# Optimization experiments

Measured on AMD Instinct MI355X. Metric: run time of the kernel, lower is better.

Reference implementation:

```python
import jax, jax.numpy as jnp
import numpy as np

B, N, K = 4, 2048, 48
NUM_RBF = 16
NUM_PE = 16
MAX_REL = 32
EDGE_C = 128
PE_IN = 2 * MAX_REL + 2  # 66


def setup_inputs() -> dict:
    key = jax.random.key(0)
    ks = jax.random.split(key, 10)
    coords = jax.random.normal(ks[0], (B, N, 3), dtype=jnp.float32) * 10.0
    token_exists_mask = jnp.ones((B, N), dtype=jnp.float32)
    token_bonds = (jax.random.uniform(ks[1], (B, N, N)) < 0.01).astype(jnp.float32)
    pe_w = jax.random.normal(ks[2], (PE_IN, NUM_PE), dtype=jnp.float32) * 0.05
    pe_b = jnp.zeros((NUM_PE,), dtype=jnp.float32)
    edge_w = jax.random.normal(ks[3], (NUM_PE + NUM_RBF + 1, EDGE_C), dtype=jnp.float32) * 0.05
    ln_g = jnp.ones((EDGE_C,), dtype=jnp.float32)
    ln_b = jnp.zeros((EDGE_C,), dtype=jnp.float32)
    token_to_center_atom = jax.random.randint(ks[4], (B, N), 0, N, dtype=jnp.int32)
    residue_index = jnp.sort(jax.random.randint(ks[5], (B, N), 0, 4096, dtype=jnp.int32), axis=-1)
    asym_id = jax.random.randint(ks[6], (B, N), 0, 4, dtype=jnp.int32)
    is_ligand = jax.random.randint(ks[7], (B, N), 0, 2, dtype=jnp.int32)
    return {
        'coords': coords, 'token_exists_mask': token_exists_mask,
        'token_bonds': token_bonds, 'pe_w': pe_w, 'pe_b': pe_b,
        'edge_w': edge_w, 'ln_g': ln_g, 'ln_b': ln_b,
        'token_to_center_atom': token_to_center_atom,
        'residue_index': residue_index, 'asym_id': asym_id,
        'is_ligand': is_ligand,
    }


def _gather_edges(M, E_idx):
    # M: [B, N, N], E_idx: [B, N, K] -> [B, N, K]
    return jnp.take_along_axis(M, E_idx, axis=2)


def _rbf(D):
    # D: [..., K] -> [..., K, NUM_RBF]
    D_mu = jnp.linspace(2.0, 22.0, NUM_RBF)
    D_sigma = (22.0 - 2.0) / NUM_RBF
    return jnp.exp(-(((D[..., None] - D_mu) / D_sigma) ** 2))


def reference(coords, token_exists_mask, token_bonds, pe_w, pe_b, edge_w,
              ln_g, ln_b, token_to_center_atom, residue_index, asym_id, is_ligand):
    # token coords: center atom per token, masked
    X = jnp.take_along_axis(coords, token_to_center_atom[..., None], axis=1)
    X = X * token_exists_mask[..., None]  # [B, N, 3]

    # masked pairwise distances + KNN (smallest K, sorted ascending)
    mask = token_exists_mask
    mask_2d = mask[:, None, :] * mask[:, :, None]  # [B, N, N]
    dX = X[:, :, None, :] - X[:, None, :, :]
    D = mask_2d * jnp.sqrt(jnp.sum(dX * dX, axis=-1) + 1e-6)
    D_max = jnp.max(D, axis=-1, keepdims=True)
    D_adjust = D + (1.0 - mask_2d) * D_max
    neg_D, E_idx = jax.lax.top_k(-D_adjust, K)  # largest of -D == smallest of D
    D_neighbors = -neg_D  # [B, N, K]

    RBF_all = _rbf(D_neighbors)  # [B, N, K, NUM_RBF]

    # relative sequence position features
    offset = residue_index[:, :, None] - residue_index[:, None, :]  # [B, N, N]
    offset_e = _gather_edges(offset, E_idx)  # [B, N, K]
    chain_labels = jnp.zeros_like(asym_id)  # use_multichain_encoding=False
    d_chains = (chain_labels[:, :, None] - chain_labels[:, None, :] == 0).astype(jnp.int32)
    E_chains = _gather_edges(d_chains, E_idx)  # [B, N, K]
    d = jnp.clip(offset_e + MAX_REL, 0, 2 * MAX_REL) * E_chains + (1 - E_chains) * (2 * MAX_REL + 1)
    d_onehot = jax.nn.one_hot(d, PE_IN, dtype=jnp.float32)
    E_positional = d_onehot @ pe_w + pe_b  # [B, N, K, NUM_PE]

    # ligand-gated bond feature
    lig = is_ligand.astype(bool)
    tb_mask = (lig[:, :, None] | lig[:, None, :]).astype(token_bonds.dtype)
    tb = token_bonds * tb_mask
    tb_e = _gather_edges(tb, E_idx)[..., None]  # [B, N, K, 1]

    # fuse, embed, layernorm
    E = jnp.concatenate([E_positional, RBF_all, tb_e], axis=-1)  # [B, N, K, 33]
    E = E @ edge_w  # [B, N, K, EDGE_C]
    mu = jnp.mean(E, axis=-1, keepdims=True)
    var = jnp.mean((E - mu) ** 2, axis=-1, keepdims=True)
    E = (E - mu) / jnp.sqrt(var + 1e-5) * ln_g + ln_b
    return (E, E_idx, D_neighbors)
```

## Files before the change

kernel.cpp:

```cpp
#include <hip/hip_runtime.h>
#include <math.h>

namespace {
constexpr int B_ = 4;
constexpr int N_ = 2048;
constexpr int K_ = 48;
constexpr int MAX_REL_ = 32;
constexpr int EDGE_C_ = 128;
constexpr int NUM_PE_ = 16;
constexpr int NROWS = B_ * N_;
constexpr int NEDGE = NROWS * K_;
}

__global__ __launch_bounds__(256) void x_kernel(const float* __restrict__ coords,
                                                const float* __restrict__ mask,
                                                const int* __restrict__ t2ca,
                                                float* __restrict__ X) {
    int r = blockIdx.x * 256 + threadIdx.x;
    if (r >= NROWS) return;
    int b = r >> 11;
    int c = t2ca[r];
    float m = mask[r];
    const float* s = coords + ((size_t)(b * N_ + c)) * 3;
    X[r * 3 + 0] = __fmul_rn(s[0], m);
    X[r * 3 + 1] = __fmul_rn(s[1], m);
    X[r * 3 + 2] = __fmul_rn(s[2], m);
}

__global__ __launch_bounds__(256) void prep_a(const float* __restrict__ edge_w,
                                              const float* __restrict__ ln_g,
                                              float* __restrict__ Wcf,
                                              float* __restrict__ Wg) {
    __shared__ float sm[33];
    const int wv = threadIdx.x >> 6;
    const int lane = threadIdx.x & 63;
    for (int r = wv; r < 33; r += 4) {
        float v = edge_w[r * 128 + lane] + edge_w[r * 128 + 64 + lane];
        #pragma unroll
        for (int off = 32; off; off >>= 1) v += __shfl_xor(v, off, 64);
        if (lane == 0) sm[r] = v * (1.0f / 128.0f);
    }
    __syncthreads();
    for (int idx = threadIdx.x; idx < 33 * 128; idx += 256) {
        int p = idx >> 7, c = idx & 127;
        float cen = edge_w[idx] - sm[p];
        Wcf[idx] = cen;
        if (p >= 16) Wg[(p - 16) * 128 + c] = cen * ln_g[c];
    }
}

__global__ __launch_bounds__(128) void prep_b(const float* __restrict__ pe_w,
                                              const float* __restrict__ pe_b,
                                              const float* __restrict__ Wcf,
                                              const float* __restrict__ ln_g,
                                              float* __restrict__ C1c,
                                              float* __restrict__ C1g) {
    const int d = blockIdx.x, c = threadIdx.x;
    float acc = 0.0f;
    #pragma unroll
    for (int q = 0; q < 16; ++q)
        acc = fmaf(pe_w[d * 16 + q] + pe_b[q], Wcf[q * 128 + c], acc);
    C1c[d * 128 + c] = acc;
    C1g[d * 128 + c] = acc * ln_g[c];
}

__global__ __launch_bounds__(256) void prep_c(const float* __restrict__ Wcf,
                                              const float* __restrict__ C1c,
                                              float* __restrict__ V0,
                                              float* __restrict__ T12_2,
                                              float* __restrict__ Tb1_2,
                                              float* __restrict__ A22,
                                              float* __restrict__ A23_2,
                                              float* __restrict__ A33) {
    const int idx = blockIdx.x * 256 + threadIdx.x;
    const float* u; const float* v; float scale; float* dst;
    if (idx < 1040) {
        int d = idx >> 4, r = idx & 15;
        u = C1c + d * 128; v = Wcf + (16 + r) * 128;
        scale = 2.0f / 128.0f; dst = T12_2 + idx;
    } else if (idx < 1105) {
        int d = idx - 1040;
        u = C1c + d * 128; v = u; scale = 1.0f / 128.0f; dst = V0 + d;
    } else if (idx < 1170) {
        int d = idx - 1105;
        u = C1c + d * 128; v = Wcf + 32 * 128; scale = 2.0f / 128.0f; dst = Tb1_2 + d;
    } else if (idx < 1426) {
        int i = idx - 1170; int r = i >> 4, s = i & 15;
        u = Wcf + (16 + r) * 128; v = Wcf + (16 + s) * 128;
        scale = 1.0f / 128.0f; dst = A22 + i;
    } else if (idx < 1442) {
        int r = idx - 1426;
        u = Wcf + (16 + r) * 128; v = Wcf + 32 * 128;
        scale = 2.0f / 128.0f; dst = A23_2 + r;
    } else if (idx == 1442) {
        u = Wcf + 32 * 128; v = u; scale = 1.0f / 128.0f; dst = A33;
    } else return;
    float a = 0.0f;
    #pragma unroll 8
    for (int c = 0; c < 128; ++c) a = fmaf(u[c], v[c], a);
    *dst = a * scale;
}

__global__ __launch_bounds__(256) void knn_kernel(const float* __restrict__ X,
                                                  const float* __restrict__ mask,
                                                  float* __restrict__ eidx_f,
                                                  float* __restrict__ dneb) {
    __shared__ unsigned s_hist[4][256];
    __shared__ unsigned long long s_cbuf[4][64];
    const int wv = threadIdx.x >> 6;
    const int lane = threadIdx.x & 63;
    const int row = blockIdx.x * 4 + wv;
    const int b = row >> 11;

    const float xi0 = X[row * 3 + 0];
    const float xi1 = X[row * 3 + 1];
    const float xi2 = X[row * 3 + 2];
    const float mi = mask[row];
    const float* Xb = X + (size_t)b * N_ * 3;
    const float* mb = mask + b * N_;

    unsigned fb[32];
    float lmax = -INFINITY;
    #pragma unroll
    for (int t = 0; t < 32; ++t) {
        int j = t * 64 + lane;
        float dx = __fsub_rn(xi0, Xb[j * 3 + 0]);
        float dy = __fsub_rn(xi1, Xb[j * 3 + 1]);
        float dz = __fsub_rn(xi2, Xb[j * 3 + 2]);
        float d2 = __fmaf_rn(dz, dz, __fmaf_rn(dx, dx, __fmul_rn(dy, dy)));
        float m2 = __fmul_rn(mi, mb[j]);
        float dd = __fmul_rn(m2, __fsqrt_rn(__fadd_rn(d2, 1e-6f)));
        fb[t] = __float_as_uint(dd);
        lmax = fmaxf(lmax, dd);
    }
    #pragma unroll
    for (int off = 32; off; off >>= 1) lmax = fmaxf(lmax, __shfl_xor(lmax, off, 64));

    unsigned fmin_l = 0xFFFFFFFFu, fmax_l = 0u;
    #pragma unroll
    for (int t = 0; t < 32; ++t) {
        int j = t * 64 + lane;
        float m2 = __fmul_rn(mi, mb[j]);
        float adj = __fadd_rn(__uint_as_float(fb[t]),
                              __fmul_rn(__fsub_rn(1.0f, m2), lmax));
        unsigned u = __float_as_uint(adj);
        fb[t] = u;
        fmin_l = min(fmin_l, u);
        fmax_l = max(fmax_l, u);
    }
    #pragma unroll
    for (int off = 32; off; off >>= 1) {
        fmin_l = min(fmin_l, (unsigned)__shfl_xor((int)fmin_l, off, 64));
        fmax_l = max(fmax_l, (unsigned)__shfl_xor((int)fmax_l, off, 64));
    }
    const unsigned fminb = fmin_l;
    const unsigned range = fmax_l - fminb;
    const int vbits = (range == 0u) ? 0 : (32 - __clz((int)range));
    const int L = vbits + 11;
    int sh = (L > 8) ? (L - 8) : 0;

    unsigned cand = 0xFFFFFFFFu;
    int k_rem = K_;
    unsigned long long T = 0ull;

    while (true) {
        s_hist[wv][4 * lane + 0] = 0u;
        s_hist[wv][4 * lane + 1] = 0u;
        s_hist[wv][4 * lane + 2] = 0u;
        s_hist[wv][4 * lane + 3] = 0u;
        __asm__ volatile("s_waitcnt lgkmcnt(0)" ::: "memory");
        #pragma unroll
        for (int t = 0; t < 32; ++t) {
            if ((cand >> t) & 1u) {
                unsigned dig;
                if (sh >= 11) {
                    dig = ((fb[t] - fminb) >> (sh - 11)) & 255u;
                } else {
                    unsigned long long key =
                        ((unsigned long long)(fb[t] - fminb) << 11)
                        | (unsigned long long)(unsigned)(t * 64 + lane);
                    dig = (unsigned)(key >> sh) & 255u;
                }
                atomicAdd(&s_hist[wv][dig], 1u);
            }
        }
        __asm__ volatile("s_waitcnt lgkmcnt(0)" ::: "memory");
        const unsigned c0 = s_hist[wv][4 * lane + 0];
        const unsigned c1 = s_hist[wv][4 * lane + 1];
        const unsigned c2 = s_hist[wv][4 * lane + 2];
        const unsigned c3 = s_hist[wv][4 * lane + 3];
        const unsigned s4 = c0 + c1 + c2 + c3;
        unsigned inc = s4;
        #pragma unroll
        for (int off = 1; off < 64; off <<= 1) {
            unsigned o = (unsigned)__shfl_up((int)inc, off, 64);
            if (lane >= off) inc += o;
        }
        const unsigned ex = inc - s4;
        const unsigned e1 = ex + c0, e2 = e1 + c1, e3 = e2 + c2;
        const unsigned kr = (unsigned)k_rem;
        int digl = -1; unsigned below = 0u, bc = 0u;
        if (ex < kr && kr <= e1)           { digl = 4 * lane + 0; below = ex; bc = c0; }
        else if (e1 < kr && kr <= e2)      { digl = 4 * lane + 1; below = e1; bc = c1; }
        else if (e2 < kr && kr <= e3)      { digl = 4 * lane + 2; below = e2; bc = c2; }
        else if (e3 < kr && kr <= e3 + c3) { digl = 4 * lane + 3; below = e3; bc = c3; }

        unsigned long long bal = __ballot(digl >= 0);
        int src = __ffsll((long long)bal) - 1;
        const int dstar = __shfl(digl, src, 64);
        below = (unsigned)__shfl((int)below, src, 64);
        bc    = (unsigned)__shfl((int)bc, src, 64);
        k_rem -= (int)below;

        unsigned nc = 0u;
        unsigned long long myT = 0ull;
        #pragma unroll
        for (int t = 0; t < 32; ++t) {
            if ((cand >> t) & 1u) {
                unsigned dig;
                unsigned long long key =
                    ((unsigned long long)(fb[t] - fminb) << 11)
                    | (unsigned long long)(unsigned)(t * 64 + lane);
                if (sh >= 11) dig = ((fb[t] - fminb) >> (sh - 11)) & 255u;
                else          dig = (unsigned)(key >> sh) & 255u;
                if (dig == (unsigned)dstar) { nc |= (1u << t); myT = key; }
            }
        }
        cand = nc;
        if (bc == 1u || sh == 0) {
            unsigned long long b2 = __ballot(cand != 0u);
            int owner = __ffsll((long long)b2) - 1;
            T = __shfl(myT, owner, 64);
            break;
        }
        sh = (sh > 8) ? (sh - 8) : 0;
    }

    const unsigned Tv = (unsigned)(T >> 11);
    const unsigned Tj = (unsigned)(T & 2047u);
    unsigned selm = 0u; int scnt = 0;
    #pragma unroll
    for (int t = 0; t < 32; ++t) {
        unsigned v = fb[t] - fminb;
        unsigned j = (unsigned)(t * 64 + lane);
        if (v < Tv || (v == Tv && j <= Tj)) { selm |= (1u << t); ++scnt; }
    }
    int isc = scnt;
    #pragma unroll
    for (int off = 1; off < 64; off <<= 1) {
        int o = __shfl_up(isc, off, 64);
        if (lane >= off) isc += o;
    }
    int pos = isc - scnt;
    #pragma unroll
    for (int t = 0; t < 32; ++t) {
        if ((selm >> t) & 1u) {
            s_cbuf[wv][pos] = ((unsigned long long)(fb[t] - fminb) << 11)
                            | (unsigned long long)(unsigned)(t * 64 + lane);
            ++pos;
        }
    }
    __asm__ volatile("s_waitcnt lgkmcnt(0)" ::: "memory");
    unsigned long long kk = (lane < K_) ? s_cbuf[wv][lane] : ~0ull;

    #pragma unroll
    for (int k2 = 2; k2 <= 64; k2 <<= 1) {
        #pragma unroll
        for (int j = k2 >> 1; j > 0; j >>= 1) {
            unsigned long long o = __shfl_xor(kk, j, 64);
            const bool dirAsc = ((lane & k2) == 0);
            const bool lower = ((lane & j) == 0);
            unsigned long long mn = (kk < o) ? kk : o;
            unsigned long long mx = (kk < o) ? o : kk;
            kk = (lower == dirAsc) ? mn : mx;
        }
    }

    if (lane < K_) {
        unsigned fbits = (unsigned)(kk >> 11) + fminb;
        unsigned ji = (unsigned)(kk & 2047u);
        dneb[(size_t)row * K_ + lane] = __uint_as_float(fbits);
        eidx_f[(size_t)row * K_ + lane] = (float)ji;
    }
}

__global__ __launch_bounds__(256, 3) void edge_kernel(const float* __restrict__ eidx_f,
                                                      const float* __restrict__ dneb,
                                                      const float* __restrict__ token_bonds,
                                                      const float* __restrict__ C1g,
                                                      const float* __restrict__ Wg,
                                                      const float* __restrict__ V0,
                                                      const float* __restrict__ T12_2,
                                                      const float* __restrict__ Tb1_2,
                                                      const float* __restrict__ A22,
                                                      const float* __restrict__ A23_2,
                                                      const float* __restrict__ A33,
                                                      const float* __restrict__ ln_b,
                                                      const int* __restrict__ res_idx,
                                                      const int* __restrict__ is_lig,
                                                      float* __restrict__ Eout) {
    __shared__ float s_rbf[4][K_][20];
    __shared__ float4 s_meta[4][K_];
    __shared__ float s_D[4][K_];
    __shared__ float s_A22[256];
    __shared__ float s_A23[16];
    __shared__ float s_A33v;
    const int tid = threadIdx.x;
    const int wv = tid >> 6;
    const int lane = tid & 63;
    const int row = blockIdx.x * 4 + wv;
    const int b = row >> 11;

    s_A22[tid] = A22[tid];
    if (tid < 16) s_A23[tid] = A23_2[tid];
    if (tid == 0) s_A33v = A33[0];

    const int ri = res_idx[row];
    const int li = is_lig[row];

    int doff_l = 0; float tb_l = 0.0f;
    if (lane < K_) {
        const int e = row * K_ + lane;
        const int j = (int)(eidx_f[e] + 0.5f);
        const float D = dneb[e];
        const int jrow = b * N_ + j;
        const int rj = res_idx[jrow];
        const int lj = is_lig[jrow];
        float tb = token_bonds[(size_t)row * N_ + j];
        tb_l = (li | lj) ? tb : 0.0f;
        doff_l = min(max(ri - rj + MAX_REL_, 0), 2 * MAX_REL_);
        s_D[wv][lane] = D;
    }
    __syncthreads();

    #pragma unroll
    for (int t = 0; t < (K_ * NUM_PE_) / 64; ++t) {
        const int idx = t * 64 + lane;
        const int k = idx >> 4, r = idx & 15;
        const float D = s_D[wv][k];
        const float mu = 2.0f + (float)r * (4.0f / 3.0f);
        const float x = (D - mu) * 0.8f;
        s_rbf[wv][k][r] = __expf(-x * x);
    }
    __syncthreads();

    if (lane < K_) {
        float rr[16];
        const float* rb = &s_rbf[wv][lane][0];
        *(float4*)&rr[0]  = *(const float4*)&rb[0];
        *(float4*)&rr[4]  = *(const float4*)&rb[4];
        *(float4*)&rr[8]  = *(const float4*)&rb[8];
        *(float4*)&rr[12] = *(const float4*)&rb[12];
        float var = V0[doff_l];
        const float4* t12 = (const float4*)(T12_2 + doff_l * 16);
        float4 q0 = t12[0], q1 = t12[1], q2 = t12[2], q3 = t12[3];
        var = fmaf(rr[0], q0.x, var);  var = fmaf(rr[1], q0.y, var);
        var = fmaf(rr[2], q0.z, var);  var = fmaf(rr[3], q0.w, var);
        var = fmaf(rr[4], q1.x, var);  var = fmaf(rr[5], q1.y, var);
        var = fmaf(rr[6], q1.z, var);  var = fmaf(rr[7], q1.w, var);
        var = fmaf(rr[8], q2.x, var);  var = fmaf(rr[9], q2.y, var);
        var = fmaf(rr[10], q2.z, var); var = fmaf(rr[11], q2.w, var);
        var = fmaf(rr[12], q3.x, var); var = fmaf(rr[13], q3.y, var);
        var = fmaf(rr[14], q3.z, var); var = fmaf(rr[15], q3.w, var);
        #pragma unroll
        for (int r = 0; r < 16; ++r) {
            float tr = 0.0f;
            const float4* arow = (const float4*)&s_A22[r * 16];
            #pragma unroll
            for (int s4 = 0; s4 < 4; ++s4) {
                float4 a = arow[s4];
                tr = fmaf(rr[s4 * 4 + 0], a.x, tr);
                tr = fmaf(rr[s4 * 4 + 1], a.y, tr);
                tr = fmaf(rr[s4 * 4 + 2], a.z, tr);
                tr = fmaf(rr[s4 * 4 + 3], a.w, tr);
            }
            var = fmaf(rr[r], tr, var);
        }
        if (tb_l != 0.0f) {
            float extra = Tb1_2[doff_l];
            #pragma unroll
            for (int r = 0; r < 16; ++r) extra = fmaf(rr[r], s_A23[r], extra);
            var = fmaf(tb_l, extra, var);
            var = fmaf(tb_l * tb_l, s_A33v, var);
        }
        const float rstd = rsqrtf(var + 1e-5f);
        s_meta[wv][lane] = make_float4((float)doff_l, tb_l, rstd, 0.0f);
    }
    __syncthreads();

    const int hl = lane & 31;
    const int eo = lane >> 5;
    float4 wgt[17];
    #pragma unroll
    for (int p = 0; p < 17; ++p)
        wgt[p] = ((const float4*)Wg)[p * 32 + hl];
    const float4 bb = ((const float4*)ln_b)[hl];

    float4* outp = (float4*)Eout + (size_t)row * K_ * 32 + hl;
    #pragma unroll 2
    for (int k = 0; k < K_; k += 2) {
        const float4 mt = s_meta[wv][k + eo];
        const int doffk = (int)mt.x;
        const float tbk = mt.y;
        const float rstd = mt.z;
        const float4 c1 = ((const float4*)(C1g + ((size_t)doffk << 7)))[hl];

        float rr[16];
        const float* rb = &s_rbf[wv][k + eo][0];
        *(float4*)&rr[0]  = *(const float4*)&rb[0];
        *(float4*)&rr[4]  = *(const float4*)&rb[4];
        *(float4*)&rr[8]  = *(const float4*)&rb[8];
        *(float4*)&rr[12] = *(const float4*)&rb[12];

        float ax = c1.x, ay = c1.y, az = c1.z, aw = c1.w;
        #pragma unroll
        for (int p = 0; p < 16; ++p) {
            ax = fmaf(rr[p], wgt[p].x, ax);
            ay = fmaf(rr[p], wgt[p].y, ay);
            az = fmaf(rr[p], wgt[p].z, az);
            aw = fmaf(rr[p], wgt[p].w, aw);
        }
        if (__any(tbk != 0.0f)) {
            ax = fmaf(tbk, wgt[16].x, ax);
            ay = fmaf(tbk, wgt[16].y, ay);
            az = fmaf(tbk, wgt[16].z, az);
            aw = fmaf(tbk, wgt[16].w, aw);
        }
        float4 o;
        o.x = fmaf(ax, rstd, bb.x);
        o.y = fmaf(ay, rstd, bb.y);
        o.z = fmaf(az, rstd, bb.z);
        o.w = fmaf(aw, rstd, bb.w);
        outp[(size_t)(k + eo) * 32] = o;
    }
}

extern "C" void kernel_launch(void* const* d_in, const int* in_sizes, int n_in,
                              void* d_out, int out_size, void* d_ws, size_t ws_size,
                              hipStream_t stream) {
    const float* coords      = (const float*)d_in[0];
    const float* mask        = (const float*)d_in[1];
    const float* token_bonds = (const float*)d_in[2];
    const float* pe_w        = (const float*)d_in[3];
    const float* pe_b        = (const float*)d_in[4];
    const float* edge_w      = (const float*)d_in[5];
    const float* ln_g        = (const float*)d_in[6];
    const float* ln_b        = (const float*)d_in[7];
    const int*   t2ca        = (const int*)d_in[8];
    const int*   res_idx     = (const int*)d_in[9];
    const int*   is_lig      = (const int*)d_in[11];

    float* out    = (float*)d_out;
    float* Eout   = out;
    float* eidx_f = out + (size_t)NEDGE * EDGE_C_;
    float* dneb   = eidx_f + NEDGE;

    float* X     = (float*)d_ws;
    float* Wcf   = X + (size_t)NROWS * 3;
    float* Wg    = Wcf + 33 * 128;
    float* C1c   = Wg + 17 * 128;
    float* C1g   = C1c + 65 * 128;
    float* V0    = C1g + 65 * 128;
    float* T12_2 = V0 + 65;
    float* Tb1_2 = T12_2 + 65 * 16;
    float* A22   = Tb1_2 + 65;
    float* A23_2 = A22 + 256;
    float* A33   = A23_2 + 16;

    hipLaunchKernelGGL(x_kernel, dim3(NROWS / 256), dim3(256), 0, stream,
                       coords, mask, t2ca, X);
    hipLaunchKernelGGL(prep_a, dim3(1), dim3(256), 0, stream,
                       edge_w, ln_g, Wcf, Wg);
    hipLaunchKernelGGL(prep_b, dim3(65), dim3(128), 0, stream,
                       pe_w, pe_b, Wcf, ln_g, C1c, C1g);
    hipLaunchKernelGGL(prep_c, dim3(6), dim3(256), 0, stream,
                       Wcf, C1c, V0, T12_2, Tb1_2, A22, A23_2, A33);
    hipLaunchKernelGGL(knn_kernel, dim3(NROWS / 4), dim3(256), 0, stream,
                       X, mask, eidx_f, dneb);
    hipLaunchKernelGGL(edge_kernel, dim3(NROWS / 4), dim3(256), 0, stream,
                       eidx_f, dneb, token_bonds, C1g, Wg, V0, T12_2, Tb1_2,
                       A22, A23_2, A33, ln_b, res_idx, is_lig, Eout);
}
```

Before: 379.7 us.

## Fuse KNN and edge kernels, merge prep kernels, pack coords with mask

Merges the three single-purpose prep kernels into one single-block kernel that keeps the centered weights and positional products in shared memory. Fuses the KNN kernel with the edge embedding kernel so neighbour indices and distances stay in registers rather than being read back from global memory. Block-wide syncs are replaced by per-wave LDS waits, which is valid because each wave touches only its own row's shared slices. X is packed as float4 with the mask in .w, and the mask-adjust pass uses a bitmask instead of recomputing. The trade-off is a single-block prep kernel that may serialize, and higher register pressure in the fused kernel.

```diff
diff --git a/kernel.cpp b/kernel.cpp
--- a/kernel.cpp
+++ b/kernel.cpp
@@ -15,122 +15,139 @@
 __global__ __launch_bounds__(256) void x_kernel(const float* __restrict__ coords,
                                                 const float* __restrict__ mask,
                                                 const int* __restrict__ t2ca,
-                                                float* __restrict__ X) {
+                                                float4* __restrict__ X4) {
     int r = blockIdx.x * 256 + threadIdx.x;
     if (r >= NROWS) return;
     int b = r >> 11;
     int c = t2ca[r];
     float m = mask[r];
     const float* s = coords + ((size_t)(b * N_ + c)) * 3;
-    X[r * 3 + 0] = __fmul_rn(s[0], m);
-    X[r * 3 + 1] = __fmul_rn(s[1], m);
-    X[r * 3 + 2] = __fmul_rn(s[2], m);
+    X4[r] = make_float4(__fmul_rn(s[0], m), __fmul_rn(s[1], m),
+                        __fmul_rn(s[2], m), m);
 }
 
-__global__ __launch_bounds__(256) void prep_a(const float* __restrict__ edge_w,
-                                              const float* __restrict__ ln_g,
-                                              float* __restrict__ Wcf,
-                                              float* __restrict__ Wg) {
+__global__ __launch_bounds__(256) void prep_kernel(const float* __restrict__ pe_w,
+                                                   const float* __restrict__ pe_b,
+                                                   const float* __restrict__ edge_w,
+                                                   const float* __restrict__ ln_g,
+                                                   float* __restrict__ Wg,
+                                                   float* __restrict__ C1g,
+                                                   float* __restrict__ T12_2,
+                                                   float* __restrict__ A22,
+                                                   float* __restrict__ A23_2,
+                                                   float* __restrict__ V0,
+                                                   float* __restrict__ Tb1_2,
+                                                   float* __restrict__ A33) {
+    __shared__ float sW[33][129];
+    __shared__ float sC[65][129];
     __shared__ float sm[33];
-    const int wv = threadIdx.x >> 6;
-    const int lane = threadIdx.x & 63;
+    const int tid = threadIdx.x;
+    const int wv = tid >> 6;
+    const int lane = tid & 63;
+
+    for (int idx = tid; idx < 33 * 128; idx += 256)
+        sW[idx >> 7][idx & 127] = edge_w[idx];
+    __syncthreads();
     for (int r = wv; r < 33; r += 4) {
-        float v = edge_w[r * 128 + lane] + edge_w[r * 128 + 64 + lane];
+        float v = sW[r][lane] + sW[r][64 + lane];
         #pragma unroll
         for (int off = 32; off; off >>= 1) v += __shfl_xor(v, off, 64);
         if (lane == 0) sm[r] = v * (1.0f / 128.0f);
     }
     __syncthreads();
-    for (int idx = threadIdx.x; idx < 33 * 128; idx += 256) {
+    for (int idx = tid; idx < 33 * 128; idx += 256) {
         int p = idx >> 7, c = idx & 127;
-        float cen = edge_w[idx] - sm[p];
-        Wcf[idx] = cen;
+        float cen = sW[p][c] - sm[p];
+        sW[p][c] = cen;
         if (p >= 16) Wg[(p - 16) * 128 + c] = cen * ln_g[c];
     }
+    __syncthreads();
+    for (int idx = tid; idx < 65 * 128; idx += 256) {
+        int d = idx >> 7, c = idx & 127;
+        float acc = 0.0f;
+        #pragma unroll
+        for (int q = 0; q < 16; ++q)
+            acc = fmaf(pe_w[d * 16 + q] + pe_b[q], sW[q][c], acc);
+        sC[d][c] = acc;
+        C1g[idx] = acc * ln_g[c];
+    }
+    __syncthreads();
+    for (int idx = tid; idx < 1443; idx += 256) {
+        const float* u; const float* v; float scale; float* dst;
+        if (idx < 1040) {
+            int d = idx >> 4, r = idx & 15;
+            u = &sC[d][0]; v = &sW[16 + r][0];
+            scale = 2.0f / 128.0f; dst = T12_2 + idx;
+        } else if (idx < 1105) {
+            int d = idx - 1040;
+            u = &sC[d][0]; v = u; scale = 1.0f / 128.0f; dst = V0 + d;
+        } else if (idx < 1170) {
+            int d = idx - 1105;
+            u = &sC[d][0]; v = &sW[32][0]; scale = 2.0f / 128.0f; dst = Tb1_2 + d;
+        } else if (idx < 1426) {
+            int i = idx - 1170; int r = i >> 4, s = i & 15;
+            u = &sW[16 + r][0]; v = &sW[16 + s][0];
+            scale = 1.0f / 128.0f; dst = A22 + i;
+        } else if (idx < 1442) {
+            int r = idx - 1426;
+            u = &sW[16 + r][0]; v = &sW[32][0];
+            scale = 2.0f / 128.0f; dst = A23_2 + r;
+        } else {
+            u = &sW[32][0]; v = u; scale = 1.0f / 128.0f; dst = A33;
+        }
+        float a = 0.0f;
+        #pragma unroll 8
+        for (int c = 0; c < 128; ++c) a = fmaf(u[c], v[c], a);
+        *dst = a * scale;
+    }
 }
 
-__global__ __launch_bounds__(128) void prep_b(const float* __restrict__ pe_w,
-                                              const float* __restrict__ pe_b,
-                                              const float* __restrict__ Wcf,
-                                              const float* __restrict__ ln_g,
-                                              float* __restrict__ C1c,
-                                              float* __restrict__ C1g) {
-    const int d = blockIdx.x, c = threadIdx.x;
-    float acc = 0.0f;
-    #pragma unroll
-    for (int q = 0; q < 16; ++q)
-        acc = fmaf(pe_w[d * 16 + q] + pe_b[q], Wcf[q * 128 + c], acc);
-    C1c[d * 128 + c] = acc;
-    C1g[d * 128 + c] = acc * ln_g[c];
-}
-
-__global__ __launch_bounds__(256) void prep_c(const float* __restrict__ Wcf,
-                                              const float* __restrict__ C1c,
-                                              float* __restrict__ V0,
-                                              float* __restrict__ T12_2,
-                                              float* __restrict__ Tb1_2,
-                                              float* __restrict__ A22,
-                                              float* __restrict__ A23_2,
-                                              float* __restrict__ A33) {
-    const int idx = blockIdx.x * 256 + threadIdx.x;
-    const float* u; const float* v; float scale; float* dst;
-    if (idx < 1040) {
-        int d = idx >> 4, r = idx & 15;
-        u = C1c + d * 128; v = Wcf + (16 + r) * 128;
-        scale = 2.0f / 128.0f; dst = T12_2 + idx;
-    } else if (idx < 1105) {
-        int d = idx - 1040;
-        u = C1c + d * 128; v = u; scale = 1.0f / 128.0f; dst = V0 + d;
-    } else if (idx < 1170) {
-        int d = idx - 1105;
-        u = C1c + d * 128; v = Wcf + 32 * 128; scale = 2.0f / 128.0f; dst = Tb1_2 + d;
-    } else if (idx < 1426) {
-        int i = idx - 1170; int r = i >> 4, s = i & 15;
-        u = Wcf + (16 + r) * 128; v = Wcf + (16 + s) * 128;
-        scale = 1.0f / 128.0f; dst = A22 + i;
-    } else if (idx < 1442) {
-        int r = idx - 1426;
-        u = Wcf + (16 + r) * 128; v = Wcf + 32 * 128;
-        scale = 2.0f / 128.0f; dst = A23_2 + r;
-    } else if (idx == 1442) {
-        u = Wcf + 32 * 128; v = u; scale = 1.0f / 128.0f; dst = A33;
-    } else return;
-    float a = 0.0f;
-    #pragma unroll 8
-    for (int c = 0; c < 128; ++c) a = fmaf(u[c], v[c], a);
-    *dst = a * scale;
-}
-
-__global__ __launch_bounds__(256) void knn_kernel(const float* __restrict__ X,
-                                                  const float* __restrict__ mask,
-                                                  float* __restrict__ eidx_f,
-                                                  float* __restrict__ dneb) {
+__global__ __launch_bounds__(256, 3) void fused_kernel(const float4* __restrict__ X4,
+                                                       const float* __restrict__ token_bonds,
+                                                       const float* __restrict__ C1g,
+                                                       const float* __restrict__ Wg,
+                                                       const float* __restrict__ V0,
+                                                       const float* __restrict__ T12_2,
+                                                       const float* __restrict__ Tb1_2,
+                                                       const float* __restrict__ A22,
+                                                       const float* __restrict__ A23_2,
+                                                       const float* __restrict__ A33,
+                                                       const float* __restrict__ ln_b,
+                                                       const int* __restrict__ res_idx,
+                                                       const int* __restrict__ is_lig,
+                                                       float* __restrict__ Eout,
+                                                       float* __restrict__ eidx_f,
+                                                       float* __restrict__ dneb) {
     __shared__ unsigned s_hist[4][256];
     __shared__ unsigned long long s_cbuf[4][64];
-    const int wv = threadIdx.x >> 6;
-    const int lane = threadIdx.x & 63;
+    __shared__ float s_rbf[4][K_][20];
+    __shared__ float4 s_meta[4][K_];
+    __shared__ float s_D[4][K_];
+    const int tid = threadIdx.x;
+    const int wv = tid >> 6;
+    const int lane = tid & 63;
     const int row = blockIdx.x * 4 + wv;
     const int b = row >> 11;
 
-    const float xi0 = X[row * 3 + 0];
-    const float xi1 = X[row * 3 + 1];
-    const float xi2 = X[row * 3 + 2];
-    const float mi = mask[row];
-    const float* Xb = X + (size_t)b * N_ * 3;
-    const float* mb = mask + b * N_;
+    const float4 xi = X4[row];
+    const float mi = xi.w;
+    const float4* Xb = X4 + (size_t)b * N_;
 
     unsigned fb[32];
+    unsigned mz = 0u;
     float lmax = -INFINITY;
     #pragma unroll
     for (int t = 0; t < 32; ++t) {
-        int j = t * 64 + lane;
-        float dx = __fsub_rn(xi0, Xb[j * 3 + 0]);
-        float dy = __fsub_rn(xi1, Xb[j * 3 + 1]);
-        float dz = __fsub_rn(xi2, Xb[j * 3 + 2]);
+        const int j = t * 64 + lane;
+        const float4 p = Xb[j];
+        float dx = __fsub_rn(xi.x, p.x);
+        float dy = __fsub_rn(xi.y, p.y);
+        float dz = __fsub_rn(xi.z, p.z);
         float d2 = __fmaf_rn(dz, dz, __fmaf_rn(dx, dx, __fmul_rn(dy, dy)));
-        float m2 = __fmul_rn(mi, mb[j]);
+        float m2 = __fmul_rn(mi, p.w);
         float dd = __fmul_rn(m2, __fsqrt_rn(__fadd_rn(d2, 1e-6f)));
         fb[t] = __float_as_uint(dd);
+        if (m2 == 0.0f) mz |= (1u << t);
         lmax = fmaxf(lmax, dd);
     }
     #pragma unroll
@@ -139,10 +156,7 @@
     unsigned fmin_l = 0xFFFFFFFFu, fmax_l = 0u;
     #pragma unroll
     for (int t = 0; t < 32; ++t) {
-        int j = t * 64 + lane;
-        float m2 = __fmul_rn(mi, mb[j]);
-        float adj = __fadd_rn(__uint_as_float(fb[t]),
-                              __fmul_rn(__fsub_rn(1.0f, m2), lmax));
+        float adj = ((mz >> t) & 1u) ? lmax : __uint_as_float(fb[t]);
         unsigned u = __float_as_uint(adj);
         fb[t] = u;
         fmin_l = min(fmin_l, u);
@@ -217,10 +231,10 @@
         #pragma unroll
         for (int t = 0; t < 32; ++t) {
             if ((cand >> t) & 1u) {
-                unsigned dig;
                 unsigned long long key =
                     ((unsigned long long)(fb[t] - fminb) << 11)
                     | (unsigned long long)(unsigned)(t * 64 + lane);
+                unsigned dig;
                 if (sh >= 11) dig = ((fb[t] - fminb) >> (sh - 11)) & 255u;
                 else          dig = (unsigned)(key >> sh) & 255u;
                 if (dig == (unsigned)dstar) { nc |= (1u << t); myT = key; }
@@ -276,62 +290,24 @@
         }
     }
 
-    if (lane < K_) {
-        unsigned fbits = (unsigned)(kk >> 11) + fminb;
-        unsigned ji = (unsigned)(kk & 2047u);
-        dneb[(size_t)row * K_ + lane] = __uint_as_float(fbits);
-        eidx_f[(size_t)row * K_ + lane] = (float)ji;
-    }
-}
-
-__global__ __launch_bounds__(256, 3) void edge_kernel(const float* __restrict__ eidx_f,
-                                                      const float* __restrict__ dneb,
-                                                      const float* __restrict__ token_bonds,
-                                                      const float* __restrict__ C1g,
-                                                      const float* __restrict__ Wg,
-                                                      const float* __restrict__ V0,
-                                                      const float* __restrict__ T12_2,
-                                                      const float* __restrict__ Tb1_2,
-                                                      const float* __restrict__ A22,
-                                                      const float* __restrict__ A23_2,
-                                                      const float* __restrict__ A33,
-                                                      const float* __restrict__ ln_b,
-                                                      const int* __restrict__ res_idx,
-                                                      const int* __restrict__ is_lig,
-                                                      float* __restrict__ Eout) {
-    __shared__ float s_rbf[4][K_][20];
-    __shared__ float4 s_meta[4][K_];
-    __shared__ float s_D[4][K_];
-    __shared__ float s_A22[256];
-    __shared__ float s_A23[16];
-    __shared__ float s_A33v;
-    const int tid = threadIdx.x;
-    const int wv = tid >> 6;
-    const int lane = tid & 63;
-    const int row = blockIdx.x * 4 + wv;
-    const int b = row >> 11;
-
-    s_A22[tid] = A22[tid];
-    if (tid < 16) s_A23[tid] = A23_2[tid];
-    if (tid == 0) s_A33v = A33[0];
-
     const int ri = res_idx[row];
     const int li = is_lig[row];
-
     int doff_l = 0; float tb_l = 0.0f;
     if (lane < K_) {
-        const int e = row * K_ + lane;
-        const int j = (int)(eidx_f[e] + 0.5f);
-        const float D = dneb[e];
-        const int jrow = b * N_ + j;
+        const unsigned fbits = (unsigned)(kk >> 11) + fminb;
+        const unsigned ji = (unsigned)(kk & 2047u);
+        const float D = __uint_as_float(fbits);
+        dneb[(size_t)row * K_ + lane] = D;
+        eidx_f[(size_t)row * K_ + lane] = (float)ji;
+        s_D[wv][lane] = D;
+        const int jrow = b * N_ + (int)ji;
         const int rj = res_idx[jrow];
         const int lj = is_lig[jrow];
-        float tb = token_bonds[(size_t)row * N_ + j];
+        float tb = token_bonds[(size_t)row * N_ + ji];
         tb_l = (li | lj) ? tb : 0.0f;
         doff_l = min(max(ri - rj + MAX_REL_, 0), 2 * MAX_REL_);
-        s_D[wv][lane] = D;
-    }
-    __syncthreads();
+    }
+    __asm__ volatile("s_waitcnt lgkmcnt(0)" ::: "memory");
 
     #pragma unroll
     for (int t = 0; t < (K_ * NUM_PE_) / 64; ++t) {
@@ -342,7 +318,7 @@
         const float x = (D - mu) * 0.8f;
         s_rbf[wv][k][r] = __expf(-x * x);
     }
-    __syncthreads();
+    __asm__ volatile("s_waitcnt lgkmcnt(0)" ::: "memory");
 
     if (lane < K_) {
         float rr[16];
@@ -364,8 +340,8 @@
         var = fmaf(rr[14], q3.z, var); var = fmaf(rr[15], q3.w, var);
         #pragma unroll
         for (int r = 0; r < 16; ++r) {
+            const float4* arow = (const float4*)(A22 + r * 16);
             float tr = 0.0f;
-            const float4* arow = (const float4*)&s_A22[r * 16];
             #pragma unroll
             for (int s4 = 0; s4 < 4; ++s4) {
                 float4 a = arow[s4];
@@ -379,14 +355,14 @@
         if (tb_l != 0.0f) {
             float extra = Tb1_2[doff_l];
             #pragma unroll
-            for (int r = 0; r < 16; ++r) extra = fmaf(rr[r], s_A23[r], extra);
+            for (int r = 0; r < 16; ++r) extra = fmaf(rr[r], A23_2[r], extra);
             var = fmaf(tb_l, extra, var);
-            var = fmaf(tb_l * tb_l, s_A33v, var);
+            var = fmaf(tb_l * tb_l, A33[0], var);
         }
         const float rstd = rsqrtf(var + 1e-5f);
         s_meta[wv][lane] = make_float4((float)doff_l, tb_l, rstd, 0.0f);
     }
-    __syncthreads();
+    __asm__ volatile("s_waitcnt lgkmcnt(0)" ::: "memory");
 
     const int hl = lane & 31;
     const int eo = lane >> 5;
@@ -455,29 +431,21 @@
     float* eidx_f = out + (size_t)NEDGE * EDGE_C_;
     float* dneb   = eidx_f + NEDGE;
 
-    float* X     = (float*)d_ws;
-    float* Wcf   = X + (size_t)NROWS * 3;
-    float* Wg    = Wcf + 33 * 128;
-    float* C1c   = Wg + 17 * 128;
-    float* C1g   = C1c + 65 * 128;
-    float* V0    = C1g + 65 * 128;
-    float* T12_2 = V0 + 65;
-    float* Tb1_2 = T12_2 + 65 * 16;
-    float* A22   = Tb1_2 + 65;
-    float* A23_2 = A22 + 256;
-    float* A33   = A23_2 + 16;
+    float4* X4  = (float4*)d_ws;
+    float* Wg   = (float*)d_ws + (size_t)NROWS * 4;
+    float* C1g  = Wg + 17 * 128;
+    float* T12  = C1g + 65 * 128;
+    float* A22  = T12 + 1040;
+    float* A23  = A22 + 256;
+    float* V0   = A23 + 16;
+    float* Tb1  = V0 + 65;
+    float* A33  = Tb1 + 65;
 
     hipLaunchKernelGGL(x_kernel, dim3(NROWS / 256), dim3(256), 0, stream,
-                       coords, mask, t2ca, X);
-    hipLaunchKernelGGL(prep_a, dim3(1), dim3(256), 0, stream,
-                       edge_w, ln_g, Wcf, Wg);
-    hipLaunchKernelGGL(prep_b, dim3(65), dim3(128), 0, stream,
-                       pe_w, pe_b, Wcf, ln_g, C1c, C1g);
-    hipLaunchKernelGGL(prep_c, dim3(6), dim3(256), 0, stream,
-                       Wcf, C1c, V0, T12_2, Tb1_2, A22, A23_2, A33);
-    hipLaunchKernelGGL(knn_kernel, dim3(NROWS / 4), dim3(256), 0, stream,
-                       X, mask, eidx_f, dneb);
-    hipLaunchKernelGGL(edge_kernel, dim3(NROWS / 4), dim3(256), 0, stream,
-                       eidx_f, dneb, token_bonds, C1g, Wg, V0, T12_2, Tb1_2,
-                       A22, A23_2, A33, ln_b, res_idx, is_lig, Eout);
+                       coords, mask, t2ca, X4);
+    hipLaunchKernelGGL(prep_kernel, dim3(1), dim3(256), 0, stream,
+                       pe_w, pe_b, edge_w, ln_g, Wg, C1g, T12, A22, A23, V0, Tb1, A33);
+    hipLaunchKernelGGL(fused_kernel, dim3(NROWS / 4), dim3(256), 0, stream,
+                       X4, token_bonds, C1g, Wg, V0, T12, Tb1, A22, A23, A33,
+                       ln_b, res_idx, is_lig, Eout, eidx_f, dneb);
 }
```

New measurement: 499.8 us. +31.6%, slower.
